# Optimization experiments

Measured on AMD Instinct MI355X. Metric: run time of the kernel, lower is better.

Reference implementation:

```python
import jax, jax.numpy as jnp
import numpy as np

HIDDEN = 1024
N_HEADS = 16
HEAD_DIM = HIDDEN // N_HEADS
B, S = 4, 4096


def setup_inputs() -> dict:
    key = jax.random.key(0)
    k1, k2, k3, k4, k5 = jax.random.split(key, 5)
    hidden_states = jax.random.normal(k1, (B, S, HIDDEN), dtype=jnp.float32)
    attention_mask = jnp.zeros((B, 1, 1, S), dtype=jnp.float32)
    scale = 1.0 / np.sqrt(HIDDEN)
    Wq = jax.random.normal(k2, (HIDDEN, HIDDEN), dtype=jnp.float32) * scale
    bq = jax.random.normal(k3, (HIDDEN,), dtype=jnp.float32) * 0.01
    Wkv = jax.random.normal(k4, (HIDDEN, HIDDEN), dtype=jnp.float32) * scale
    bkv = jax.random.normal(k5, (HIDDEN,), dtype=jnp.float32) * 0.01
    return {"hidden_states": hidden_states, "attention_mask": attention_mask,
            "Wq": Wq, "bq": bq, "Wkv": Wkv, "bkv": bkv}


def _split_heads(x, b, s):
    # [B, S, HIDDEN] -> [B, H, S, D]
    return x.reshape(b, s, N_HEADS, HEAD_DIM).transpose(0, 2, 1, 3)


def reference(hidden_states, attention_mask, Wq, bq, Wkv, bkv):
    b, s, _ = hidden_states.shape
    inv_sqrt_d = 1.0 / np.sqrt(HEAD_DIM)

    q = _split_heads(hidden_states @ Wq + bq, b, s)     # [B,H,S,D]
    k = _split_heads(hidden_states @ Wkv + bkv, b, s)   # [B,H,S,D]; value == key

    # ---- global token (index 0) attends to everything ----
    gq = q[:, :, 0:1, :]                                              # [B,H,1,D]
    g_scores = jnp.einsum('bhqd,bhkd->bhqk', gq, k) * inv_sqrt_d + attention_mask
    g_attn = jax.nn.softmax(g_scores, axis=-1)                        # [B,H,1,S]
    g_vec = jnp.einsum('bhqk,bhkd->bhqd', g_attn, k)                  # [B,H,1,D]

    # ---- local tokens 1..S-1: keys = [self, global_vec, prev, next(wrap to 0)] ----
    k_self = k[:, :, 1:, :]                                           # [B,H,S-1,D]
    k_glob = jnp.broadcast_to(g_vec, k_self.shape)                    # [B,H,S-1,D]
    k_prev = k[:, :, :-1, :]                                          # [B,H,S-1,D]
    k_next = jnp.concatenate([k[:, :, 2:, :], k[:, :, 0:1, :]], axis=2)
    keys4 = jnp.stack([k_self, k_glob, k_prev, k_next], axis=-1)      # [B,H,S-1,D,4]

    l_scores = jnp.einsum('bhsd,bhsdk->bhsk', q[:, :, 1:, :], keys4) * inv_sqrt_d
    l_attn = jax.nn.softmax(l_scores, axis=-1)                        # [B,H,S-1,4]
    l_vec = jnp.einsum('bhsk,bhsdk->bhsd', l_attn, keys4)             # [B,H,S-1,D]

    context = jnp.concatenate([g_vec, l_vec], axis=2)                 # [B,H,S,D]
    context = context.transpose(0, 2, 1, 3).reshape(b, s, N_HEADS * HEAD_DIM)
    return context, l_attn[:, :, :, None, :]                          # [B,H,S-1,1,4]
```

## Files before the change

### kernel.cpp

```cpp
#include <hip/hip_runtime.h>
#include <hip/hip_bf16.h>

#define NHEADS 16
#define HDIM   64
#define HID    1024
#define BB     4
#define SS     4096
#define MM     (BB*SS)
#define KK     HID
#define NN     (2*HID)

using short8 = __attribute__((ext_vector_type(8))) short;
using f32x4  = __attribute__((ext_vector_type(4))) float;

__device__ __forceinline__ float bf2f(ushort u) {
  return __uint_as_float(((unsigned)u) << 16);
}
__device__ __forceinline__ ushort f2bf(float f) {
  unsigned u = __float_as_uint(f);
  unsigned r = (u + 0x7fffu + ((u >> 16) & 1u)) >> 16;
  return (ushort)r;
}

__device__ __forceinline__ void gload16(const void* g, void* l) {
  __builtin_amdgcn_global_load_lds(
      (const __attribute__((address_space(1))) void*)g,
      (__attribute__((address_space(3))) void*)l, 16, 0, 0);
}

__global__ __launch_bounds__(256) void cast_hs_k(const float* __restrict__ in,
                                                 ushort* __restrict__ out) {
  size_t i = ((size_t)blockIdx.x * 256 + threadIdx.x) * 8;
  float4 a = *(const float4*)(in + i);
  float4 b = *(const float4*)(in + i + 4);
  ushort r[8];
  r[0]=f2bf(a.x); r[1]=f2bf(a.y); r[2]=f2bf(a.z); r[3]=f2bf(a.w);
  r[4]=f2bf(b.x); r[5]=f2bf(b.y); r[6]=f2bf(b.z); r[7]=f2bf(b.w);
  *(uint4*)(out + i) = *(const uint4*)r;
}

__global__ __launch_bounds__(256) void wcast_k(const float* __restrict__ Wq,
                                               const float* __restrict__ Wkv,
                                               ushort* __restrict__ Bt) {
  __shared__ float tile[32][33];
  int k0 = blockIdx.x * 32, n0 = blockIdx.y * 32;
  int tx = threadIdx.x, ty = threadIdx.y;
  const float* src = (n0 < HID) ? Wq : Wkv;
  int nc = (n0 < HID) ? n0 : n0 - HID;
#pragma unroll
  for (int j = 0; j < 4; ++j)
    tile[ty + 8*j][tx] = src[(size_t)(k0 + ty + 8*j) * HID + nc + tx];
  __syncthreads();
#pragma unroll
  for (int j = 0; j < 4; ++j)
    Bt[(size_t)(n0 + ty + 8*j) * KK + k0 + tx] = f2bf(tile[tx][ty + 8*j]);
}

__global__ __launch_bounds__(256) void gemm_k(const ushort* __restrict__ A,
                                              const ushort* __restrict__ Bt,
                                              const float* __restrict__ bq,
                                              const float* __restrict__ bkv,
                                              ushort* __restrict__ C) {
  __shared__ __align__(16) ushort lds[2 * 128 * 64];
  ushort* As = lds;
  ushort* Bs = lds + 128 * 64;

  const int tid = threadIdx.x;
  const int tn = blockIdx.x, tm = blockIdx.y;
  const int w = tid >> 6, lane = tid & 63;
  const int wr = w >> 1, wc = w & 1;
  const int lr = lane & 15;
  const int hi = lane >> 4;

  const ushort* Ab = A  + (size_t)tm * 128 * KK;
  const ushort* Bb = Bt + (size_t)tn * 128 * KK;

  const ushort* gp[8];
#pragma unroll
  for (int i = 0; i < 8; ++i) {
    int o  = i * 4096 + w * 1024 + lane * 16;
    int oo = o & 16383;
    int row = oo >> 7;
    int chunk = (oo >> 4) & 7;
    gp[i] = ((i < 4) ? Ab : Bb) + (size_t)row * KK + ((chunk ^ (row & 7)) << 3);
  }

  f32x4 acc[4][4];
#pragma unroll
  for (int m = 0; m < 4; ++m)
#pragma unroll
    for (int n = 0; n < 4; ++n) acc[m][n] = (f32x4){0.f, 0.f, 0.f, 0.f};

  for (int kt = 0; kt < KK / 64; ++kt) {
    __syncthreads();
#pragma unroll
    for (int i = 0; i < 8; ++i)
      gload16(gp[i], (char*)lds + i * 4096 + w * 1024);
#pragma unroll
    for (int i = 0; i < 8; ++i) gp[i] += 64;
    __syncthreads();

#pragma unroll
    for (int kk = 0; kk < 64; kk += 32) {
      const int cbase = (kk >> 3) + hi;
      short8 af[4], bfv[4];
#pragma unroll
      for (int m = 0; m < 4; ++m) {
        int row = wr * 64 + m * 16 + lr;
        af[m] = *(const short8*)((const char*)As + row * 128 +
                                 ((cbase ^ (row & 7)) << 4));
      }
#pragma unroll
      for (int n = 0; n < 4; ++n) {
        int row = wc * 64 + n * 16 + lr;
        bfv[n] = *(const short8*)((const char*)Bs + row * 128 +
                                  ((cbase ^ (row & 7)) << 4));
      }
#pragma unroll
      for (int m = 0; m < 4; ++m)
#pragma unroll
        for (int n = 0; n < 4; ++n)
          acc[m][n] = __builtin_amdgcn_mfma_f32_16x16x32_bf16(af[m], bfv[n],
                                                              acc[m][n], 0, 0, 0);
    }
  }

  __syncthreads();
  const int rr = hi * 4;
#pragma unroll
  for (int n = 0; n < 4; ++n) {
    int coll = wc * 64 + n * 16 + lr;
    int colg = tn * 128 + coll;
    float bias = (colg < HID) ? bq[colg] : bkv[colg - HID];
#pragma unroll
    for (int m = 0; m < 4; ++m) {
      int row0 = wr * 64 + m * 16 + rr;
#pragma unroll
      for (int t = 0; t < 4; ++t) {
        int rowt = row0 + t;
        *(ushort*)((char*)lds + rowt * 256 + ((coll * 2) ^ ((rowt & 7) << 4))) =
            f2bf(acc[m][n][t] + bias);
      }
    }
  }
  __syncthreads();
#pragma unroll
  for (int i = 0; i < 8; ++i) {
    int idx = i * 256 + tid;
    int row = idx >> 4, l16 = idx & 15;
    uint4 v = *(const uint4*)((const char*)lds + row * 256 +
                              ((l16 ^ (row & 7)) << 4));
    *(uint4*)(C + (size_t)(tm * 128 + row) * NN + tn * 128 + l16 * 8) = v;
  }
}

#define GCH 8
#define GCS (SS / GCH)

__global__ __launch_bounds__(512) void gattn_part_k(const ushort* __restrict__ QK,
                                                    const float* __restrict__ mask,
                                                    float* __restrict__ P) {
  const int bh = blockIdx.x >> 3, c = blockIdx.x & 7;
  const int b = bh >> 4, h = bh & 15;
  const int tid = threadIdx.x, w = tid >> 6, lane = tid & 63;
  __shared__ float sc[GCS];
  __shared__ float red[8];
  __shared__ float vacc[8][64];

  const float gq = bf2f(QK[(size_t)b * SS * NN + h * HDIM + lane]);
  const int s0 = c * GCS;
  float mx = -1e30f;
  for (int s = w; s < GCS; s += 8) {
    float kv = bf2f(QK[((size_t)b * SS + s0 + s) * NN + HID + h * HDIM + lane]);
    float p = gq * kv;
#pragma unroll
    for (int o = 32; o; o >>= 1) p += __shfl_xor(p, o, 64);
    p = p * 0.125f + mask[b * SS + s0 + s];
    if (lane == 0) sc[s] = p;
    mx = fmaxf(mx, p);
  }
  if (lane == 0) red[w] = mx;
  __syncthreads();
  float bm = -1e30f;
#pragma unroll
  for (int i = 0; i < 8; ++i) bm = fmaxf(bm, red[i]);
  __syncthreads();
  float ls = 0.f;
  for (int s = tid; s < GCS; s += 512) {
    float e = __expf(sc[s] - bm);
    sc[s] = e;
    ls += e;
  }
#pragma unroll
  for (int o = 32; o; o >>= 1) ls += __shfl_xor(ls, o, 64);
  if (lane == 0) red[w] = ls;
  __syncthreads();
  float tot = 0.f;
#pragma unroll
  for (int i = 0; i < 8; ++i) tot += red[i];

  float a = 0.f;
  for (int s = w; s < GCS; s += 8)
    a += sc[s] * bf2f(QK[((size_t)b * SS + s0 + s) * NN + HID + h * HDIM + lane]);
  vacc[w][lane] = a;
  __syncthreads();
  if (w == 0) {
    float v = 0.f;
#pragma unroll
    for (int i = 0; i < 8; ++i) v += vacc[i][lane];
    P[1024 + (bh * 8 + c) * 64 + lane] = v;
    if (lane == 0) {
      P[bh * 8 + c] = bm;
      P[512 + bh * 8 + c] = tot;
    }
  }
}

__global__ __launch_bounds__(64) void gattn_comb_k(const float* __restrict__ P,
                                                   float* __restrict__ ctx,
                                                   float* __restrict__ gvec) {
  const int bh = blockIdx.x, b = bh >> 4, h = bh & 15;
  const int lane = threadIdx.x;
  float pm[8];
  float m = -1e30f;
#pragma unroll
  for (int c = 0; c < 8; ++c) { pm[c] = P[bh * 8 + c]; m = fmaxf(m, pm[c]); }
  float tot = 0.f, g = 0.f;
#pragma unroll
  for (int c = 0; c < 8; ++c) {
    float e = __expf(pm[c] - m);
    tot += P[512 + bh * 8 + c] * e;
    g += P[1024 + (bh * 8 + c) * 64 + lane] * e;
  }
  g /= tot;
  gvec[b * HID + h * HDIM + lane] = g;
  ctx[(size_t)b * SS * HID + h * HDIM + lane] = g;
}

__device__ __forceinline__ void unpack16(const ushort* __restrict__ p, float* f) {
  uint4 v0 = *(const uint4*)p;
  uint4 v1 = *(const uint4*)(p + 8);
  unsigned u[8] = {v0.x, v0.y, v0.z, v0.w, v1.x, v1.y, v1.z, v1.w};
#pragma unroll
  for (int i = 0; i < 8; ++i) {
    f[2*i]   = __uint_as_float(u[i] << 16);
    f[2*i+1] = __uint_as_float(u[i] & 0xffff0000u);
  }
}

__global__ __launch_bounds__(256) void local_attn_k(const ushort* __restrict__ QK,
                                                    const float* __restrict__ gvec,
                                                    float* __restrict__ out) {
  const int blk = blockIdx.x;
  const int b = blk >> 10;
  const int s = 1 + ((blk & 1023) << 2) + (int)(threadIdx.x >> 6);
  if (s >= SS) return;
  const int lane = threadIdx.x & 63;
  const int g = lane >> 2, j = lane & 3;
  const int db = g*HDIM + j*16;

  const size_t base = ((size_t)b*SS + s) * NN;
  const ushort* qp  = QK + base + db;
  const ushort* ksp = QK + base + HID + db;
  const ushort* kpp = QK + base - NN + HID + db;
  const int sn = (s == SS-1) ? 0 : s + 1;
  const ushort* knp = QK + ((size_t)b*SS + sn)*NN + HID + db;
  const float*  gvp = gvec + b*HID + db;

  float q[16], ks[16], kp[16], kn[16], gv[16];
  unpack16(qp, q); unpack16(ksp, ks); unpack16(kpp, kp); unpack16(knp, kn);
#pragma unroll
  for (int t = 0; t < 16; t += 4) *(float4*)(gv + t) = *(const float4*)(gvp + t);

  float d0=0.f, d1=0.f, d2=0.f, d3=0.f;
#pragma unroll
  for (int t = 0; t < 16; ++t) {
    d0 += q[t]*ks[t]; d1 += q[t]*gv[t]; d2 += q[t]*kp[t]; d3 += q[t]*kn[t];
  }
  d0 += __shfl_xor(d0, 1, 64); d0 += __shfl_xor(d0, 2, 64);
  d1 += __shfl_xor(d1, 1, 64); d1 += __shfl_xor(d1, 2, 64);
  d2 += __shfl_xor(d2, 1, 64); d2 += __shfl_xor(d2, 2, 64);
  d3 += __shfl_xor(d3, 1, 64); d3 += __shfl_xor(d3, 2, 64);

  float s0 = d0*0.125f, s1 = d1*0.125f, s2 = d2*0.125f, s3 = d3*0.125f;
  float m = fmaxf(fmaxf(s0, s1), fmaxf(s2, s3));
  float e0 = __expf(s0 - m), e1 = __expf(s1 - m), e2 = __expf(s2 - m), e3 = __expf(s3 - m);
  float inv = 1.f / (e0 + e1 + e2 + e3);
  float a0 = e0*inv, a1 = e1*inv, a2 = e2*inv, a3 = e3*inv;

  float o[16];
#pragma unroll
  for (int t = 0; t < 16; ++t) o[t] = a0*ks[t] + a1*gv[t] + a2*kp[t] + a3*kn[t];
  float* cp = out + ((size_t)b*SS + s)*HID + db;
#pragma unroll
  for (int t = 0; t < 16; t += 4) *(float4*)(cp + t) = *(const float4*)(o + t);

  if (j == 0) {
    float4 av; av.x = a0; av.y = a1; av.z = a2; av.w = a3;
    *(float4*)(out + (size_t)BB*SS*HID + (((size_t)b*NHEADS + g)*(SS-1) + (s-1))*4) = av;
  }
}

extern "C" void kernel_launch(void* const* d_in, const int* in_sizes, int n_in,
                              void* d_out, int out_size, void* d_ws, size_t ws_size,
                              hipStream_t stream) {
  const float* hs   = (const float*)d_in[0];
  const float* mask = (const float*)d_in[1];
  const float* Wq   = (const float*)d_in[2];
  const float* bq   = (const float*)d_in[3];
  const float* Wkv  = (const float*)d_in[4];
  const float* bkv  = (const float*)d_in[5];
  float* out = (float*)d_out;

  char* ws = (char*)d_ws;
  ushort* hsb  = (ushort*)ws;
  ushort* Bt   = (ushort*)(ws + 33554432);
  ushort* QK   = (ushort*)(ws + 33554432 + 4194304);
  float*  gvec = (float*)(ws + 33554432 + 4194304 + 67108864);
  float*  P    = (float*)(ws + 33554432 + 4194304 + 67108864 + 16384);

  cast_hs_k<<<MM*KK/(256*8), 256, 0, stream>>>(hs, hsb);
  wcast_k<<<dim3(KK/32, NN/32), dim3(32, 8), 0, stream>>>(Wq, Wkv, Bt);
  gemm_k<<<dim3(NN/128, MM/128), 256, 0, stream>>>(hsb, Bt, bq, bkv, QK);
  gattn_part_k<<<BB*NHEADS*GCH, 512, 0, stream>>>(QK, mask, P);
  gattn_comb_k<<<BB*NHEADS, 64, 0, stream>>>(P, out, gvec);
  local_attn_k<<<BB*1024, 256, 0, stream>>>(QK, gvec, out);
}
```

Before: 180.7 us.

## Rewrite projection GEMM with 256x256 tiles, double-buffered LDS and ping-pong scheduling

The QK projection GEMM moves from 128x128 tiles with 4 waves to 256x256 tiles with 8 waves and 128KB of dynamic LDS. Global-to-LDS loads for the next K tile are interleaved between MFMA phases, using manual barriers, s_setprio and explicit vmcnt waits. A block-index remap groups blocks for L2 reuse. This is meant to hide load latency and raise arithmetic intensity, at the cost of heavy LDS and register use and fragile hand-scheduled synchronisation.

```diff
diff --git a/kernel.cpp b/kernel.cpp
--- a/kernel.cpp
+++ b/kernel.cpp
@@ -56,101 +56,135 @@
     Bt[(size_t)(n0 + ty + 8*j) * KK + k0 + tx] = f2bf(tile[tx][ty + 8*j]);
 }
 
-__global__ __launch_bounds__(256) void gemm_k(const ushort* __restrict__ A,
-                                              const ushort* __restrict__ Bt,
-                                              const float* __restrict__ bq,
-                                              const float* __restrict__ bkv,
-                                              ushort* __restrict__ C) {
-  __shared__ __align__(16) ushort lds[2 * 128 * 64];
-  ushort* As = lds;
-  ushort* Bs = lds + 128 * 64;
-
+__global__ __launch_bounds__(512, 2) void gemm_k(const ushort* __restrict__ A,
+                                                 const ushort* __restrict__ Bt,
+                                                 const float* __restrict__ bq,
+                                                 const float* __restrict__ bkv,
+                                                 ushort* __restrict__ C) {
+  extern __shared__ char lds_c[];
   const int tid = threadIdx.x;
-  const int tn = blockIdx.x, tm = blockIdx.y;
+  const int bid = blockIdx.x;
+  const int wg = (bid & 7) * 64 + (bid >> 3);
+  const int tm = wg >> 3, tn = wg & 7;
   const int w = tid >> 6, lane = tid & 63;
-  const int wr = w >> 1, wc = w & 1;
-  const int lr = lane & 15;
-  const int hi = lane >> 4;
-
-  const ushort* Ab = A  + (size_t)tm * 128 * KK;
-  const ushort* Bb = Bt + (size_t)tn * 128 * KK;
-
-  const ushort* gp[8];
-#pragma unroll
-  for (int i = 0; i < 8; ++i) {
-    int o  = i * 4096 + w * 1024 + lane * 16;
-    int oo = o & 16383;
-    int row = oo >> 7;
-    int chunk = (oo >> 4) & 7;
-    gp[i] = ((i < 4) ? Ab : Bb) + (size_t)row * KK + ((chunk ^ (row & 7)) << 3);
-  }
-
-  f32x4 acc[4][4];
-#pragma unroll
-  for (int m = 0; m < 4; ++m)
-#pragma unroll
-    for (int n = 0; n < 4; ++n) acc[m][n] = (f32x4){0.f, 0.f, 0.f, 0.f};
-
-  for (int kt = 0; kt < KK / 64; ++kt) {
-    __syncthreads();
-#pragma unroll
-    for (int i = 0; i < 8; ++i)
-      gload16(gp[i], (char*)lds + i * 4096 + w * 1024);
-#pragma unroll
-    for (int i = 0; i < 8; ++i) gp[i] += 64;
-    __syncthreads();
-
-#pragma unroll
-    for (int kk = 0; kk < 64; kk += 32) {
-      const int cbase = (kk >> 3) + hi;
-      short8 af[4], bfv[4];
-#pragma unroll
-      for (int m = 0; m < 4; ++m) {
-        int row = wr * 64 + m * 16 + lr;
-        af[m] = *(const short8*)((const char*)As + row * 128 +
-                                 ((cbase ^ (row & 7)) << 4));
-      }
-#pragma unroll
-      for (int n = 0; n < 4; ++n) {
-        int row = wc * 64 + n * 16 + lr;
-        bfv[n] = *(const short8*)((const char*)Bs + row * 128 +
-                                  ((cbase ^ (row & 7)) << 4));
-      }
-#pragma unroll
-      for (int m = 0; m < 4; ++m)
-#pragma unroll
-        for (int n = 0; n < 4; ++n)
-          acc[m][n] = __builtin_amdgcn_mfma_f32_16x16x32_bf16(af[m], bfv[n],
-                                                              acc[m][n], 0, 0, 0);
-    }
-  }
-
-  __syncthreads();
-  const int rr = hi * 4;
+  const int wr = w >> 2, wc = w & 3;
+  const int lr = lane & 15, hi = lane >> 4;
+
+  const ushort* Ab = A  + (size_t)tm * 256 * KK;
+  const ushort* Bb = Bt + (size_t)tn * 256 * KK;
+
+  const int o0 = tid * 16;
+  const int srow = tid >> 3;
+  const int sc = tid & 7;
+  const size_t aoff = (size_t)srow * KK + ((sc ^ (srow & 7)) << 3);
+
+  const int swz0 = (hi ^ (lr & 7)) << 4;
+  const int swz1 = ((4 + hi) ^ (lr & 7)) << 4;
+  const int rowA = (wr * 128 + lr) * 128;
+  const int rowB = (wc * 64 + lr) * 128;
+
+  float biasv[4];
 #pragma unroll
   for (int n = 0; n < 4; ++n) {
-    int coll = wc * 64 + n * 16 + lr;
-    int colg = tn * 128 + coll;
-    float bias = (colg < HID) ? bq[colg] : bkv[colg - HID];
-#pragma unroll
-    for (int m = 0; m < 4; ++m) {
-      int row0 = wr * 64 + m * 16 + rr;
+    int col = tn * 256 + wc * 64 + n * 16 + lr;
+    biasv[n] = (col < HID) ? bq[col] : bkv[col - HID];
+  }
+
+  f32x4 acc[8][4];
+#pragma unroll
+  for (int M = 0; M < 8; ++M)
+#pragma unroll
+    for (int n = 0; n < 4; ++n) acc[M][n] = (f32x4){0.f, 0.f, 0.f, 0.f};
+  short8 bfrag[4];
+
+#define STG(PANEL, TILE, DST)                                                   \
+  {                                                                             \
+    const ushort* g0_ = (PANEL) + (TILE) * 64 + aoff;                           \
+    gload16(g0_,         lds_c + (DST) + o0);                                   \
+    gload16(g0_ + 65536, lds_c + (DST) + 8192 + o0);                            \
+  }
+
+#define LOADB(BUFB, SWZ)                                                        \
+  _Pragma("unroll") for (int n = 0; n < 4; ++n)                                 \
+    bfrag[n] = *(const short8*)(lds_c + (BUFB) + rowB + n * 2048 + (SWZ));
+
+#define CPH(BUFA, MH, SWZ, STAGE_CODE, TAIL_CODE)                               \
+  {                                                                             \
+    short8 afrag[4];                                                            \
+    _Pragma("unroll") for (int m = 0; m < 4; ++m)                               \
+      afrag[m] = *(const short8*)(lds_c + (BUFA) + rowA + (MH) * 8192 +         \
+                                  m * 2048 + (SWZ));                            \
+    STAGE_CODE;                                                                 \
+    __builtin_amdgcn_s_barrier();                                               \
+    asm volatile("" ::: "memory");                                              \
+    __builtin_amdgcn_s_setprio(1);                                              \
+    _Pragma("unroll") for (int m = 0; m < 4; ++m)                               \
+      _Pragma("unroll") for (int n = 0; n < 4; ++n)                             \
+        acc[(MH) * 4 + m][n] = __builtin_amdgcn_mfma_f32_16x16x32_bf16(         \
+            afrag[m], bfrag[n], acc[(MH) * 4 + m][n], 0, 0, 0);                 \
+    __builtin_amdgcn_s_setprio(0);                                              \
+    TAIL_CODE;                                                                  \
+    __builtin_amdgcn_s_barrier();                                               \
+    asm volatile("" ::: "memory");                                              \
+  }
+
+  STG(Bb,          0, 32768);
+  STG(Bb + 131072, 0, 49152);
+  STG(Ab,          0, 0);
+  STG(Ab + 131072, 0, 16384);
+  STG(Bb,          1, 98304);
+  asm volatile("s_waitcnt vmcnt(2)" ::: "memory");
+  __builtin_amdgcn_s_barrier();
+  asm volatile("" ::: "memory");
+
+#define ITER_BODY(T1, TN0, TN1, G, VM4)                                          \
+  LOADB(32768, swz0);                                                            \
+  CPH(0, 0, swz0, STG(Bb + 131072, (T1), 114688), {});                           \
+  CPH(0, 1, swz0, STG(Ab, (T1), 65536), {});                                     \
+  LOADB(32768, swz1);                                                            \
+  CPH(0, 0, swz1, STG(Ab + 131072, (T1), 81920), {});                            \
+  CPH(0, 1, swz1, { if (G) STG(Bb, (TN0), 32768) },                              \
+      { asm volatile("s_waitcnt vmcnt(" #VM4 ")" ::: "memory");                  \
+        __builtin_amdgcn_sched_barrier(0); });                                   \
+  LOADB(98304, swz0);                                                            \
+  CPH(65536, 0, swz0, { if (G) STG(Bb + 131072, (TN0), 49152) }, {});            \
+  CPH(65536, 1, swz0, { if (G) STG(Ab, (TN0), 0) }, {});                         \
+  LOADB(98304, swz1);                                                            \
+  CPH(65536, 0, swz1, { if (G) STG(Ab + 131072, (TN0), 16384) }, {});            \
+  CPH(65536, 1, swz1, { if (G) STG(Bb, (TN1), 98304) },                          \
+      { asm volatile("s_waitcnt vmcnt(2)" ::: "memory");                         \
+        __builtin_amdgcn_sched_barrier(0); });
+
+  for (int it = 0; it < 7; ++it) {
+    ITER_BODY(2 * it + 1, 2 * it + 2, 2 * it + 3, true, 2)
+  }
+  ITER_BODY(15, 0, 0, false, 0)
+
+#undef ITER_BODY
+#undef CPH
+#undef LOADB
+#undef STG
+
+#pragma unroll
+  for (int M = 0; M < 8; ++M) {
+#pragma unroll
+    for (int n = 0; n < 4; ++n) {
 #pragma unroll
       for (int t = 0; t < 4; ++t) {
-        int rowt = row0 + t;
-        *(ushort*)((char*)lds + rowt * 256 + ((coll * 2) ^ ((rowt & 7) << 4))) =
-            f2bf(acc[m][n][t] + bias);
+        int row = wr * 128 + M * 16 + hi * 4 + t;
+        int col = wc * 64 + n * 16 + lr;
+        *(ushort*)(lds_c + row * 512 + ((col * 2) ^ ((row & 7) << 4))) =
+            f2bf(acc[M][n][t] + biasv[n]);
       }
     }
   }
   __syncthreads();
 #pragma unroll
-  for (int i = 0; i < 8; ++i) {
-    int idx = i * 256 + tid;
-    int row = idx >> 4, l16 = idx & 15;
-    uint4 v = *(const uint4*)((const char*)lds + row * 256 +
-                              ((l16 ^ (row & 7)) << 4));
-    *(uint4*)(C + (size_t)(tm * 128 + row) * NN + tn * 128 + l16 * 8) = v;
+  for (int i = 0; i < 16; ++i) {
+    int idx = i * 512 + tid;
+    int row = idx >> 5, l = idx & 31;
+    uint4 v = *(const uint4*)(lds_c + row * 512 + ((l ^ (row & 7)) << 4));
+    *(uint4*)(C + (size_t)(tm * 256 + row) * NN + tn * 256 + l * 8) = v;
   }
 }
 
@@ -321,7 +355,7 @@
 
   cast_hs_k<<<MM*KK/(256*8), 256, 0, stream>>>(hs, hsb);
   wcast_k<<<dim3(KK/32, NN/32), dim3(32, 8), 0, stream>>>(Wq, Wkv, Bt);
-  gemm_k<<<dim3(NN/128, MM/128), 256, 0, stream>>>(hsb, Bt, bq, bkv, QK);
+  gemm_k<<<dim3((MM/256)*(NN/256)), dim3(512), 131072, stream>>>(hsb, Bt, bq, bkv, QK);
   gattn_part_k<<<BB*NHEADS*GCH, 512, 0, stream>>>(QK, mask, P);
   gattn_comb_k<<<BB*NHEADS, 64, 0, stream>>>(P, out, gvec);
   local_attn_k<<<BB*1024, 256, 0, stream>>>(QK, gvec, out);
```

Measured after the change: 170.0 us. 5.9% less time.
